# Optimization experiments

Measured on AMD Instinct MI355X. Metric: run time of the kernel, lower is better.

The kernel has to match this reference:

```python
import jax, jax.numpy as jnp
import numpy as np

D = 1024
HEADS = 16
HD = D // HEADS


def setup_inputs() -> dict:
    key = jax.random.key(0)
    kx, kqkv, kout = jax.random.split(key, 3)
    x = jax.random.normal(kx, (2, 2048, D), dtype=jnp.float32)
    # torch Linear weight is [out, in]; store same layout
    W_qkv = jax.random.normal(kqkv, (3 * D, D), dtype=jnp.float32) * (D ** -0.5)
    W_out = jax.random.normal(kout, (D, D), dtype=jnp.float32) * (D ** -0.5)
    return {"x": x, "W_qkv": W_qkv, "W_out": W_out}


def reference(x, W_qkv, W_out):
    B, T, _ = x.shape
    scale = HD ** -0.5
    qkv = jnp.einsum('btd,ed->bte', x, W_qkv)            # [B,T,3D]
    qkv = qkv.reshape(B, T, 3, HEADS, HD)
    q = jnp.transpose(qkv[:, :, 0], (0, 2, 1, 3))        # [B,H,T,hd]
    k = jnp.transpose(qkv[:, :, 1], (0, 2, 1, 3))
    v = jnp.transpose(qkv[:, :, 2], (0, 2, 1, 3))
    attn = jnp.einsum('bhqd,bhkd->bhqk', q, k) * scale   # [B,H,T,T]
    causal = jnp.tril(jnp.ones((T, T), dtype=bool))
    attn = jnp.where(causal, attn, -jnp.inf)
    attn = jax.nn.softmax(attn, axis=-1)
    out = jnp.einsum('bhqk,bhkd->bhqd', attn, v)         # [B,H,T,hd]
    out = jnp.transpose(out, (0, 2, 1, 3)).reshape(B, T, HEADS * HD)
    return jnp.einsum('btd,ed->bte', out, W_out)
```

## Files before the change

kernel.cpp:

```cpp
#include <hip/hip_runtime.h>
#include <cmath>


typedef unsigned short u16;
typedef unsigned int u32;
typedef short short8 __attribute__((ext_vector_type(8)));
typedef float floatx4 __attribute__((ext_vector_type(4)));

#define T_SZ 2048
#define HD_SZ 64
#define QSCALE 0.1803368801111244f

__device__ __forceinline__ u16 f2bf(float f) {
  unsigned u = __float_as_uint(f);
  u += 0x7fffu + ((u >> 16) & 1u);
  return (u16)(u >> 16);
}

__device__ __forceinline__ u32 pack_bf2(float lo, float hi) {
  return __builtin_amdgcn_perm(__float_as_uint(hi), __float_as_uint(lo), 0x07060302u);
}

__device__ __forceinline__ u32 cvtpk(float a, float b) {
  u32 r;
  asm("v_cvt_pk_bf16_f32 %0, %1, %2" : "=v"(r) : "v"(a), "v"(b));
  return r;
}

__device__ __forceinline__ void pl32swap(u32& a, u32& b) {
  asm("v_permlane32_swap_b32 %0, %1" : "+v"(a), "+v"(b));
}
__device__ __forceinline__ void pl16swap(u32& a, u32& b) {
  asm("v_permlane16_swap_b32 %0, %1" : "+v"(a), "+v"(b));
}

__device__ __forceinline__ void exp4(float s0, float s1, float s2, float s3,
                                     float& p0, float& p1, float& p2, float& p3) {
  asm("v_exp_f32 %0, %4\n\t"
      "v_exp_f32 %1, %5\n\t"
      "v_exp_f32 %2, %6\n\t"
      "v_exp_f32 %3, %7\n\t"
      "s_nop 1"
      : "=&v"(p0), "=&v"(p1), "=&v"(p2), "=&v"(p3)
      : "v"(s0), "v"(s1), "v"(s2), "v"(s3));
}

__device__ __forceinline__ void gload16(const u16* g, u16* l) {
  __builtin_amdgcn_global_load_lds(
      (const __attribute__((address_space(1))) void*)g,
      (__attribute__((address_space(3))) void*)l, 16, 0, 0);
}

__global__ __launch_bounds__(256) void cast3(const float* __restrict__ a, u16* __restrict__ ao, int na4,
                                             const float* __restrict__ b, u16* __restrict__ bo, int nb4,
                                             const float* __restrict__ c, u16* __restrict__ co, int nc4) {
  int i = blockIdx.x * 256 + threadIdx.x;
  const float* src;
  u16* dst;
  int j;
  if (i < na4) { src = a; dst = ao; j = i; }
  else if (i < na4 + nb4) { src = b; dst = bo; j = i - na4; }
  else { j = i - na4 - nb4; if (j >= nc4) return; src = c; dst = co; }
  float4 f = ((const float4*)src)[j];
  ushort4 o;
  o.x = f2bf(f.x); o.y = f2bf(f.y); o.z = f2bf(f.z); o.w = f2bf(f.w);
  ((ushort4*)dst)[j] = o;
}

__global__ __launch_bounds__(256, 3) void gemm_qkv(const u16* __restrict__ A,
                                                   const u16* __restrict__ Bt,
                                                   u16* __restrict__ Qf,
                                                   u16* __restrict__ Kf,
                                                   u16* __restrict__ Vf) {
  __shared__ u16 SM[2 * 128 * 64];
  u16* As = SM;
  u16* Bs = SM + 128 * 64;
  const int Kdim = 1024;
  const int tid = threadIdx.x;
  const int lane = tid & 63;
  const int wave = tid >> 6;
  const int quad = lane >> 4;
  const int l16 = lane & 15;
  const int wm = wave >> 1, wn = wave & 1;
  const int m0 = blockIdx.y * 128;
  const int n0 = blockIdx.x * 128;

  floatx4 acc[4][4];
#pragma unroll
  for (int i = 0; i < 4; i++)
#pragma unroll
    for (int j = 0; j < 4; j++) acc[i][j] = (floatx4){0.f, 0.f, 0.f, 0.f};

  const int srow = lane >> 3;
  const int scol = ((lane & 7) ^ srow) * 8;
  const u16* gpA[4];
  const u16* gpB[4];
  u16 *lpA[4], *lpB[4];
#pragma unroll
  for (int u = 0; u < 4; u++) {
    const int row = wave * 32 + u * 8 + srow;
    gpA[u] = A + (size_t)(m0 + row) * Kdim + scol;
    gpB[u] = Bt + (size_t)(n0 + row) * Kdim + scol;
    lpA[u] = As + (wave * 32 + u * 8) * 64 + lane * 8;
    lpB[u] = Bs + (wave * 32 + u * 8) * 64 + lane * 8;
  }

  const int fsw = l16 & 7;

  for (int k0 = 0; k0 < Kdim; k0 += 64) {
    __syncthreads();
#pragma unroll
    for (int u = 0; u < 4; u++) {
      gload16(gpA[u] + k0, lpA[u]);
      gload16(gpB[u] + k0, lpB[u]);
    }
    __syncthreads();

#pragma unroll
    for (int h = 0; h < 2; h++) {
      const int seg = ((h * 4 + quad) ^ fsw) * 8;
      short8 af[4], bf[4];
#pragma unroll
      for (int mt = 0; mt < 4; mt++)
        af[mt] = *(const short8*)&As[(wm * 64 + mt * 16 + l16) * 64 + seg];
#pragma unroll
      for (int nt = 0; nt < 4; nt++)
        bf[nt] = *(const short8*)&Bs[(wn * 64 + nt * 16 + l16) * 64 + seg];
#pragma unroll
      for (int mt = 0; mt < 4; mt++)
#pragma unroll
        for (int nt = 0; nt < 4; nt++)
          acc[mt][nt] = __builtin_amdgcn_mfma_f32_16x16x32_bf16(af[mt], bf[nt], acc[mt][nt], 0, 0, 0);
    }
  }

  const int dest = n0 >> 10;
  const int n0w = n0 + wn * 64;
  const int m_abs = m0 + wm * 64;
  const int b = m_abs >> 11;
  const int t0w = m_abs & 2047;
  const int h = (n0w >> 6) & 15;
  const int bh = b * 16 + h;
  u16* dstp = (dest == 0) ? Qf : (dest == 1) ? Kf : Vf;

  auto do_epi = [&](u16* ep) {
    if (dest == 2) {
#pragma unroll
      for (int nt = 0; nt < 4; nt++) {
#pragma unroll
        for (int mt = 0; mt < 4; mt++) {
          uint2 w;
          w.x = (u32)f2bf(acc[mt][nt][0]) | ((u32)f2bf(acc[mt][nt][1]) << 16);
          w.y = (u32)f2bf(acc[mt][nt][2]) | ((u32)f2bf(acc[mt][nt][3]) << 16);
          *(uint2*)&ep[(nt * 16 + l16) * 72 + mt * 16 + quad * 4] = w;
        }
      }
    } else {
      const float sc = (dest == 0) ? QSCALE : 1.0f;
#pragma unroll
      for (int mt = 0; mt < 4; mt++)
#pragma unroll
        for (int nt = 0; nt < 4; nt++)
#pragma unroll
          for (int r = 0; r < 4; r++)
            ep[(mt * 16 + quad * 4 + r) * 72 + nt * 16 + l16] =
                f2bf(acc[mt][nt][r] * sc);
    }
#pragma unroll
    for (int blk = 0; blk < 8; blk++) {
      const int tgd = blk >> 1;
      const int half = blk & 1;
      const short8 v = *(const short8*)&ep[(tgd * 16 + l16) * 72 + half * 32 + quad * 8];
      size_t base;
      if (dest == 0)
        base = ((size_t)(bh * 128 + (t0w >> 4) + tgd) * 2 + half) * 512;
      else
        base = (((size_t)(bh * 32 + (t0w >> 6)) * 4 + tgd) * 2 + half) * 512;
      *(short8*)(dstp + base + lane * 8) = v;
    }
  };

  __syncthreads();
  if (wave < 2) do_epi(&SM[wave * 64 * 72]);
  __syncthreads();
  if (wave >= 2) do_epi(&SM[(wave - 2) * 64 * 72]);
}

__global__ __launch_bounds__(256, 4) void gemm_out(const u16* __restrict__ A,
                                                   const u16* __restrict__ Bt,
                                                   float* __restrict__ Cout) {
  __shared__ u16 As[64 * 64];
  __shared__ u16 Bs[128 * 64];
  const int Kdim = 1024;
  const int tid = threadIdx.x;
  const int lane = tid & 63;
  const int wave = tid >> 6;
  const int quad = lane >> 4;
  const int l16 = lane & 15;
  const int wm = wave >> 1, wn = wave & 1;
  const int m0 = blockIdx.y * 64;
  const int n0 = blockIdx.x * 128;

  floatx4 acc[2][4];
#pragma unroll
  for (int i = 0; i < 2; i++)
#pragma unroll
    for (int j = 0; j < 4; j++) acc[i][j] = (floatx4){0.f, 0.f, 0.f, 0.f};

  const int srow = lane >> 3;
  const int scol = ((lane & 7) ^ srow) * 8;
  const u16* gpA[2];
  const u16* gpB[4];
  u16 *lpA[2], *lpB[4];
#pragma unroll
  for (int u = 0; u < 2; u++) {
    const int row = wave * 16 + u * 8 + srow;
    gpA[u] = A + (size_t)(m0 + row) * Kdim + scol;
    lpA[u] = As + (wave * 16 + u * 8) * 64 + lane * 8;
  }
#pragma unroll
  for (int u = 0; u < 4; u++) {
    const int row = wave * 32 + u * 8 + srow;
    gpB[u] = Bt + (size_t)(n0 + row) * Kdim + scol;
    lpB[u] = Bs + (wave * 32 + u * 8) * 64 + lane * 8;
  }

  const int fsw = l16 & 7;

  for (int k0 = 0; k0 < Kdim; k0 += 64) {
    __syncthreads();
#pragma unroll
    for (int u = 0; u < 2; u++) gload16(gpA[u] + k0, lpA[u]);
#pragma unroll
    for (int u = 0; u < 4; u++) gload16(gpB[u] + k0, lpB[u]);
    __syncthreads();

#pragma unroll
    for (int h = 0; h < 2; h++) {
      const int seg = ((h * 4 + quad) ^ fsw) * 8;
      short8 af[2], bf[4];
#pragma unroll
      for (int mt = 0; mt < 2; mt++)
        af[mt] = *(const short8*)&As[(wm * 32 + mt * 16 + l16) * 64 + seg];
#pragma unroll
      for (int nt = 0; nt < 4; nt++)
        bf[nt] = *(const short8*)&Bs[(wn * 64 + nt * 16 + l16) * 64 + seg];
#pragma unroll
      for (int mt = 0; mt < 2; mt++)
#pragma unroll
        for (int nt = 0; nt < 4; nt++)
          acc[mt][nt] = __builtin_amdgcn_mfma_f32_16x16x32_bf16(af[mt], bf[nt], acc[mt][nt], 0, 0, 0);
    }
  }

#pragma unroll
  for (int mt = 0; mt < 2; mt++)
#pragma unroll
    for (int nt = 0; nt < 4; nt++)
#pragma unroll
      for (int r = 0; r < 4; r++) {
        const int m = m0 + wm * 32 + mt * 16 + quad * 4 + r;
        const int n = n0 + wn * 64 + nt * 16 + l16;
        Cout[(size_t)m * 1024 + n] = acc[mt][nt][r];
      }
}

__global__ __launch_bounds__(256, 4) void flash_attn(const u16* __restrict__ Qf,
                                                     const u16* __restrict__ Kf,
                                                     const u16* __restrict__ Vf,
                                                     u16* __restrict__ Og) {
  __shared__ __align__(16) u16 KV[2][16 * 512];
  const int tid = threadIdx.x;
  const int lane = tid & 63, wave = tid >> 6;
  const int quad = lane >> 4, l16 = lane & 15;
  const int bh = blockIdx.x;
  const int by = blockIdx.y;
  const int r = by & 7, qq = by >> 3;
  const int g = (qq == 0) ? r : (qq == 1) ? 15 - r : (qq == 2) ? 16 + r : 31 - r;
  const int b = bh >> 4, h = bh & 15;
  const u16* Qb = Qf + ((size_t)bh << 17);
  const u16* Kb = Kf + ((size_t)bh << 17);
  const u16* Vb = Vf + ((size_t)bh << 17);

  const u16* qp = Qb + ((size_t)(g * 4 + wave)) * 1024 + lane * 8;
  const short8 qf0 = *(const short8*)qp;
  const short8 qf1 = *(const short8*)(qp + 512);

  floatx4 l_acc = (floatx4){0.f, 0.f, 0.f, 0.f};
  floatx4 o_acc[4];
#pragma unroll
  for (int dt = 0; dt < 4; dt++) o_acc[dt] = (floatx4){0.f, 0.f, 0.f, 0.f};

  short8 onesf;
#pragma unroll
  for (int i = 0; i < 8; i++) onesf[i] = (short)0x3F80;

  const u16* gkv[4];
  u16* l0[4];
  u16* l1[4];
#pragma unroll
  for (int i = 0; i < 4; i++) {
    const int c = wave * 4 + i;
    gkv[i] = ((c < 8) ? (Kb + c * 512) : (Vb + (c - 8) * 512)) + lane * 8;
    l0[i] = &KV[0][c * 512] + lane * 8;
    l1[i] = &KV[1][c * 512] + lane * 8;
  }

  auto load_tile = [&](int kt, u16* const* lp) {
#pragma unroll
    for (int i = 0; i < 4; i++) gload16(gkv[i] + (size_t)kt * 4096, lp[i]);
  };

  const floatx4 zero4 = {0.f, 0.f, 0.f, 0.f};

  auto compute = [&](int kt, const u16* Kl) {
    const bool diag = (kt == g);
    short8 ka[4][2];
#pragma unroll
    for (int nt = 0; nt < 4; nt++)
#pragma unroll
      for (int hh = 0; hh < 2; hh++)
        ka[nt][hh] = *(const short8*)&Kl[(nt * 2 + hh) * 512 + lane * 8];
    floatx4 sacc[4];
    __builtin_amdgcn_s_setprio(1);
#pragma unroll
    for (int nt = 0; nt < 4; nt++) {
      if (diag && nt > wave) continue;
      floatx4 s = __builtin_amdgcn_mfma_f32_16x16x32_bf16(ka[nt][0], qf0, zero4, 0, 0, 0);
      sacc[nt] = __builtin_amdgcn_mfma_f32_16x16x32_bf16(ka[nt][1], qf1, s, 0, 0, 0);
    }
    __builtin_amdgcn_s_setprio(0);
    u32 c[4][2];
#pragma unroll
    for (int nt = 0; nt < 4; nt++) {
      float p0 = 0.f, p1 = 0.f, p2 = 0.f, p3 = 0.f;
      if (!(diag && nt > wave)) {
        exp4(sacc[nt][0], sacc[nt][1], sacc[nt][2], sacc[nt][3], p0, p1, p2, p3);
        if (diag && nt == wave) {
          if (quad * 4 + 0 > l16) p0 = 0.f;
          if (quad * 4 + 1 > l16) p1 = 0.f;
          if (quad * 4 + 2 > l16) p2 = 0.f;
          if (quad * 4 + 3 > l16) p3 = 0.f;
        }
      }
      c[nt][0] = cvtpk(p0, p1);
      c[nt][1] = cvtpk(p2, p3);
    }
    pl32swap(c[0][0], c[1][0]); pl16swap(c[0][0], c[1][0]);
    pl32swap(c[0][1], c[1][1]); pl16swap(c[0][1], c[1][1]);
    pl32swap(c[2][0], c[3][0]); pl16swap(c[2][0], c[3][0]);
    pl32swap(c[2][1], c[3][1]); pl16swap(c[2][1], c[3][1]);
    union { u32 w[4]; short8 s8; } P0, P1;
    P0.w[0] = c[0][0]; P0.w[1] = c[0][1]; P0.w[2] = c[1][0]; P0.w[3] = c[1][1];
    P1.w[0] = c[2][0]; P1.w[1] = c[2][1]; P1.w[2] = c[3][0]; P1.w[3] = c[3][1];
    const short8 pf0 = P0.s8;
    const short8 pf1 = P1.s8;
    short8 va[4][2];
#pragma unroll
    for (int dt = 0; dt < 4; dt++)
#pragma unroll
      for (int hh = 0; hh < 2; hh++)
        va[dt][hh] = *(const short8*)&Kl[4096 + (dt * 2 + hh) * 512 + lane * 8];
    const bool skip_hi = diag && (wave < 2);
    __builtin_amdgcn_s_setprio(1);
    l_acc = __builtin_amdgcn_mfma_f32_16x16x32_bf16(onesf, pf0, l_acc, 0, 0, 0);
    if (!skip_hi)
      l_acc = __builtin_amdgcn_mfma_f32_16x16x32_bf16(onesf, pf1, l_acc, 0, 0, 0);
#pragma unroll
    for (int dt = 0; dt < 4; dt++) {
      o_acc[dt] = __builtin_amdgcn_mfma_f32_16x16x32_bf16(va[dt][0], pf0, o_acc[dt], 0, 0, 0);
      if (!skip_hi)
        o_acc[dt] = __builtin_amdgcn_mfma_f32_16x16x32_bf16(va[dt][1], pf1, o_acc[dt], 0, 0, 0);
    }
    __builtin_amdgcn_s_setprio(0);
  };

  load_tile(0, l0);
  __syncthreads();
  int kt = 0;
  for (;;) {
    if (kt < g) load_tile(kt + 1, l1);
    compute(kt, &KV[0][0]);
    if (++kt > g) break;
    __syncthreads();
    if (kt < g) load_tile(kt + 1, l0);
    compute(kt, &KV[1][0]);
    if (++kt > g) break;
    __syncthreads();
  }

  const float inv_l = 1.0f / l_acc[0];
  const int t0 = g * 64 + wave * 16;
  const size_t row = ((size_t)(b * 2048 + t0 + l16) << 10) + h * 64;
#pragma unroll
  for (int dt = 0; dt < 4; dt++) {
    uint2 w;
    w.x = pack_bf2(o_acc[dt][0] * inv_l, o_acc[dt][1] * inv_l);
    w.y = pack_bf2(o_acc[dt][2] * inv_l, o_acc[dt][3] * inv_l);
    *(uint2*)&Og[row + dt * 16 + quad * 4] = w;
  }
}

extern "C" void kernel_launch(void* const* d_in, const int* in_sizes, int n_in,
                              void* d_out, int out_size, void* d_ws, size_t ws_size,
                              hipStream_t stream) {
  const float* x = (const float*)d_in[0];
  const float* Wqkv = (const float*)d_in[1];
  const float* Wout = (const float*)d_in[2];
  float* out = (float*)d_out;

  char* ws = (char*)d_ws;
  u16* xb    = (u16*)(ws + 0);
  u16* wqkvb = (u16*)(ws + 8388608);
  u16* woutb = (u16*)(ws + 14680064);
  u16* Qf    = (u16*)(ws + 16777216);
  u16* Kf    = (u16*)(ws + 25165824);
  u16* Vf    = (u16*)(ws + 33554432);
  u16* attn  = (u16*)(ws + 41943040);

  cast3<<<8192, 256, 0, stream>>>(x, xb, 1048576, Wqkv, wqkvb, 786432,
                                  Wout, woutb, 262144);

  gemm_qkv<<<dim3(24, 32), 256, 0, stream>>>(xb, wqkvb, Qf, Kf, Vf);

  flash_attn<<<dim3(32, 32), 256, 0, stream>>>(Qf, Kf, Vf, attn);

  gemm_out<<<dim3(8, 64), 256, 0, stream>>>(attn, woutb, out);
}
```

Before: 155.7 us.

## Give each attention wave two query strips; remap GEMM block order

The flash attention kernel now runs with 128 threads per block, and each wave handles two 16-row query strips. Each K/V fragment read from shared memory is therefore reused for twice as many MFMAs, and each wave issues twice as many global-to-LDS loads. Both GEMM kernels also remap block indices so that consecutive blocks are spread across XCD-style groups, aiming for better L2 locality. The trade-offs are higher register pressure per wave (launch bounds drop to 2 blocks per SM) and fewer waves available to hide latency.

```diff
diff --git a/kernel.cpp b/kernel.cpp
--- a/kernel.cpp
+++ b/kernel.cpp
@@ -82,8 +82,12 @@
   const int quad = lane >> 4;
   const int l16 = lane & 15;
   const int wm = wave >> 1, wn = wave & 1;
-  const int m0 = blockIdx.y * 128;
-  const int n0 = blockIdx.x * 128;
+  const int linear = blockIdx.y * 24 + blockIdx.x;
+  const int nb = (linear & 7) * 96 + (linear >> 3);
+  const int bxx = nb % 24;
+  const int byy = nb / 24;
+  const int m0 = byy * 128;
+  const int n0 = bxx * 128;
 
   floatx4 acc[4][4];
 #pragma unroll
@@ -198,8 +202,10 @@
   const int quad = lane >> 4;
   const int l16 = lane & 15;
   const int wm = wave >> 1, wn = wave & 1;
-  const int m0 = blockIdx.y * 64;
-  const int n0 = blockIdx.x * 128;
+  const int linear = blockIdx.y * 8 + blockIdx.x;
+  const int nb = (linear & 7) * 64 + (linear >> 3);
+  const int m0 = (nb >> 3) * 64;
+  const int n0 = (nb & 7) * 128;
 
   floatx4 acc[2][4];
 #pragma unroll
@@ -265,7 +271,7 @@
       }
 }
 
-__global__ __launch_bounds__(256, 4) void flash_attn(const u16* __restrict__ Qf,
+__global__ __launch_bounds__(128, 2) void flash_attn(const u16* __restrict__ Qf,
                                                      const u16* __restrict__ Kf,
                                                      const u16* __restrict__ Vf,
                                                      u16* __restrict__ Og) {
@@ -282,25 +288,33 @@
   const u16* Kb = Kf + ((size_t)bh << 17);
   const u16* Vb = Vf + ((size_t)bh << 17);
 
-  const u16* qp = Qb + ((size_t)(g * 4 + wave)) * 1024 + lane * 8;
-  const short8 qf0 = *(const short8*)qp;
-  const short8 qf1 = *(const short8*)(qp + 512);
-
-  floatx4 l_acc = (floatx4){0.f, 0.f, 0.f, 0.f};
-  floatx4 o_acc[4];
-#pragma unroll
-  for (int dt = 0; dt < 4; dt++) o_acc[dt] = (floatx4){0.f, 0.f, 0.f, 0.f};
+  short8 qf[2][2];
+#pragma unroll
+  for (int u = 0; u < 2; u++) {
+    const u16* qp = Qb + ((size_t)(g * 4 + wave * 2 + u)) * 1024 + lane * 8;
+    qf[u][0] = *(const short8*)qp;
+    qf[u][1] = *(const short8*)(qp + 512);
+  }
+
+  floatx4 l_acc[2];
+  floatx4 o_acc[2][4];
+#pragma unroll
+  for (int u = 0; u < 2; u++) {
+    l_acc[u] = (floatx4){0.f, 0.f, 0.f, 0.f};
+#pragma unroll
+    for (int dt = 0; dt < 4; dt++) o_acc[u][dt] = (floatx4){0.f, 0.f, 0.f, 0.f};
+  }
 
   short8 onesf;
 #pragma unroll
   for (int i = 0; i < 8; i++) onesf[i] = (short)0x3F80;
 
-  const u16* gkv[4];
-  u16* l0[4];
-  u16* l1[4];
-#pragma unroll
-  for (int i = 0; i < 4; i++) {
-    const int c = wave * 4 + i;
+  const u16* gkv[8];
+  u16* l0[8];
+  u16* l1[8];
+#pragma unroll
+  for (int i = 0; i < 8; i++) {
+    const int c = wave * 8 + i;
     gkv[i] = ((c < 8) ? (Kb + c * 512) : (Vb + (c - 8) * 512)) + lane * 8;
     l0[i] = &KV[0][c * 512] + lane * 8;
     l1[i] = &KV[1][c * 512] + lane * 8;
@@ -308,7 +322,7 @@
 
   auto load_tile = [&](int kt, u16* const* lp) {
 #pragma unroll
-    for (int i = 0; i < 4; i++) gload16(gkv[i] + (size_t)kt * 4096, lp[i]);
+    for (int i = 0; i < 8; i++) gload16(gkv[i] + (size_t)kt * 4096, lp[i]);
   };
 
   const floatx4 zero4 = {0.f, 0.f, 0.f, 0.f};
@@ -321,56 +335,66 @@
 #pragma unroll
       for (int hh = 0; hh < 2; hh++)
         ka[nt][hh] = *(const short8*)&Kl[(nt * 2 + hh) * 512 + lane * 8];
-    floatx4 sacc[4];
-    __builtin_amdgcn_s_setprio(1);
-#pragma unroll
-    for (int nt = 0; nt < 4; nt++) {
-      if (diag && nt > wave) continue;
-      floatx4 s = __builtin_amdgcn_mfma_f32_16x16x32_bf16(ka[nt][0], qf0, zero4, 0, 0, 0);
-      sacc[nt] = __builtin_amdgcn_mfma_f32_16x16x32_bf16(ka[nt][1], qf1, s, 0, 0, 0);
-    }
-    __builtin_amdgcn_s_setprio(0);
-    u32 c[4][2];
-#pragma unroll
-    for (int nt = 0; nt < 4; nt++) {
-      float p0 = 0.f, p1 = 0.f, p2 = 0.f, p3 = 0.f;
-      if (!(diag && nt > wave)) {
-        exp4(sacc[nt][0], sacc[nt][1], sacc[nt][2], sacc[nt][3], p0, p1, p2, p3);
-        if (diag && nt == wave) {
-          if (quad * 4 + 0 > l16) p0 = 0.f;
-          if (quad * 4 + 1 > l16) p1 = 0.f;
-          if (quad * 4 + 2 > l16) p2 = 0.f;
-          if (quad * 4 + 3 > l16) p3 = 0.f;
+
+    short8 pf[2][2];
+#pragma unroll
+    for (int u = 0; u < 2; u++) {
+      const int cq = wave * 2 + u;
+      floatx4 sacc[4];
+      __builtin_amdgcn_s_setprio(1);
+#pragma unroll
+      for (int nt = 0; nt < 4; nt++) {
+        if (diag && nt > cq) continue;
+        floatx4 s = __builtin_amdgcn_mfma_f32_16x16x32_bf16(ka[nt][0], qf[u][0], zero4, 0, 0, 0);
+        sacc[nt] = __builtin_amdgcn_mfma_f32_16x16x32_bf16(ka[nt][1], qf[u][1], s, 0, 0, 0);
+      }
+      __builtin_amdgcn_s_setprio(0);
+      u32 c[4][2];
+#pragma unroll
+      for (int nt = 0; nt < 4; nt++) {
+        float p0 = 0.f, p1 = 0.f, p2 = 0.f, p3 = 0.f;
+        if (!(diag && nt > cq)) {
+          exp4(sacc[nt][0], sacc[nt][1], sacc[nt][2], sacc[nt][3], p0, p1, p2, p3);
+          if (diag && nt == cq) {
+            if (quad * 4 + 0 > l16) p0 = 0.f;
+            if (quad * 4 + 1 > l16) p1 = 0.f;
+            if (quad * 4 + 2 > l16) p2 = 0.f;
+            if (quad * 4 + 3 > l16) p3 = 0.f;
+          }
         }
+        c[nt][0] = cvtpk(p0, p1);
+        c[nt][1] = cvtpk(p2, p3);
       }
-      c[nt][0] = cvtpk(p0, p1);
-      c[nt][1] = cvtpk(p2, p3);
-    }
-    pl32swap(c[0][0], c[1][0]); pl16swap(c[0][0], c[1][0]);
-    pl32swap(c[0][1], c[1][1]); pl16swap(c[0][1], c[1][1]);
-    pl32swap(c[2][0], c[3][0]); pl16swap(c[2][0], c[3][0]);
-    pl32swap(c[2][1], c[3][1]); pl16swap(c[2][1], c[3][1]);
-    union { u32 w[4]; short8 s8; } P0, P1;
-    P0.w[0] = c[0][0]; P0.w[1] = c[0][1]; P0.w[2] = c[1][0]; P0.w[3] = c[1][1];
-    P1.w[0] = c[2][0]; P1.w[1] = c[2][1]; P1.w[2] = c[3][0]; P1.w[3] = c[3][1];
-    const short8 pf0 = P0.s8;
-    const short8 pf1 = P1.s8;
+      pl32swap(c[0][0], c[1][0]); pl16swap(c[0][0], c[1][0]);
+      pl32swap(c[0][1], c[1][1]); pl16swap(c[0][1], c[1][1]);
+      pl32swap(c[2][0], c[3][0]); pl16swap(c[2][0], c[3][0]);
+      pl32swap(c[2][1], c[3][1]); pl16swap(c[2][1], c[3][1]);
+      union { u32 w[4]; short8 s8; } P0, P1;
+      P0.w[0] = c[0][0]; P0.w[1] = c[0][1]; P0.w[2] = c[1][0]; P0.w[3] = c[1][1];
+      P1.w[0] = c[2][0]; P1.w[1] = c[2][1]; P1.w[2] = c[3][0]; P1.w[3] = c[3][1];
+      pf[u][0] = P0.s8;
+      pf[u][1] = P1.s8;
+    }
     short8 va[4][2];
 #pragma unroll
     for (int dt = 0; dt < 4; dt++)
 #pragma unroll
       for (int hh = 0; hh < 2; hh++)
         va[dt][hh] = *(const short8*)&Kl[4096 + (dt * 2 + hh) * 512 + lane * 8];
-    const bool skip_hi = diag && (wave < 2);
     __builtin_amdgcn_s_setprio(1);
-    l_acc = __builtin_amdgcn_mfma_f32_16x16x32_bf16(onesf, pf0, l_acc, 0, 0, 0);
-    if (!skip_hi)
-      l_acc = __builtin_amdgcn_mfma_f32_16x16x32_bf16(onesf, pf1, l_acc, 0, 0, 0);
-#pragma unroll
-    for (int dt = 0; dt < 4; dt++) {
-      o_acc[dt] = __builtin_amdgcn_mfma_f32_16x16x32_bf16(va[dt][0], pf0, o_acc[dt], 0, 0, 0);
+#pragma unroll
+    for (int u = 0; u < 2; u++) {
+      const int cq = wave * 2 + u;
+      const bool skip_hi = diag && (cq < 2);
+      l_acc[u] = __builtin_amdgcn_mfma_f32_16x16x32_bf16(onesf, pf[u][0], l_acc[u], 0, 0, 0);
       if (!skip_hi)
-        o_acc[dt] = __builtin_amdgcn_mfma_f32_16x16x32_bf16(va[dt][1], pf1, o_acc[dt], 0, 0, 0);
+        l_acc[u] = __builtin_amdgcn_mfma_f32_16x16x32_bf16(onesf, pf[u][1], l_acc[u], 0, 0, 0);
+#pragma unroll
+      for (int dt = 0; dt < 4; dt++) {
+        o_acc[u][dt] = __builtin_amdgcn_mfma_f32_16x16x32_bf16(va[dt][0], pf[u][0], o_acc[u][dt], 0, 0, 0);
+        if (!skip_hi)
+          o_acc[u][dt] = __builtin_amdgcn_mfma_f32_16x16x32_bf16(va[dt][1], pf[u][1], o_acc[u][dt], 0, 0, 0);
+      }
     }
     __builtin_amdgcn_s_setprio(0);
   };
@@ -389,15 +413,19 @@
     __syncthreads();
   }
 
-  const float inv_l = 1.0f / l_acc[0];
-  const int t0 = g * 64 + wave * 16;
-  const size_t row = ((size_t)(b * 2048 + t0 + l16) << 10) + h * 64;
-#pragma unroll
-  for (int dt = 0; dt < 4; dt++) {
-    uint2 w;
-    w.x = pack_bf2(o_acc[dt][0] * inv_l, o_acc[dt][1] * inv_l);
-    w.y = pack_bf2(o_acc[dt][2] * inv_l, o_acc[dt][3] * inv_l);
-    *(uint2*)&Og[row + dt * 16 + quad * 4] = w;
+#pragma unroll
+  for (int u = 0; u < 2; u++) {
+    const int cq = wave * 2 + u;
+    const float inv_l = 1.0f / l_acc[u][0];
+    const int t0 = g * 64 + cq * 16;
+    const size_t row = ((size_t)(b * 2048 + t0 + l16) << 10) + h * 64;
+#pragma unroll
+    for (int dt = 0; dt < 4; dt++) {
+      uint2 w;
+      w.x = pack_bf2(o_acc[u][dt][0] * inv_l, o_acc[u][dt][1] * inv_l);
+      w.y = pack_bf2(o_acc[u][dt][2] * inv_l, o_acc[u][dt][3] * inv_l);
+      *(uint2*)&Og[row + dt * 16 + quad * 4] = w;
+    }
   }
 }
 
@@ -423,7 +451,7 @@
 
   gemm_qkv<<<dim3(24, 32), 256, 0, stream>>>(xb, wqkvb, Qf, Kf, Vf);
 
-  flash_attn<<<dim3(32, 32), 256, 0, stream>>>(Qf, Kf, Vf, attn);
+  flash_attn<<<dim3(32, 32), 128, 0, stream>>>(Qf, Kf, Vf, attn);
 
   gemm_out<<<dim3(8, 64), 256, 0, stream>>>(attn, woutb, out);
 }
```

New measurement: 161.0 us. 3.4% more time.
